# Kernel tuning notes

Hardware: AMD Instinct MI355X
Metric: run time of the kernel (lower is better)

Reference implementation:

```python
import jax, jax.numpy as jnp
import numpy as np

DIM = 1024
NUM_HEADS = 16
HEAD_DIM = DIM // NUM_HEADS
SCALE = HEAD_DIM ** -0.5
CAUSAL = True


def setup_inputs() -> dict:
    key = jax.random.key(0)
    k_x, k_qkv, k_proj, k_pb = jax.random.split(key, 4)
    B, S = 4, 2048
    x = jax.random.normal(k_x, (B, S, DIM), dtype=jnp.float32)
    # nn.Linear(dim, 3*dim, bias=False): weight [3*dim, dim]; store transposed [dim, 3*dim]
    w_qkv = jax.random.normal(k_qkv, (DIM, 3 * DIM), dtype=jnp.float32) * (DIM ** -0.5)
    w_proj = jax.random.normal(k_proj, (DIM, DIM), dtype=jnp.float32) * (DIM ** -0.5)
    b_proj = jax.random.normal(k_pb, (DIM,), dtype=jnp.float32) * 0.01
    return {"x": x, "w_qkv": w_qkv, "w_proj": w_proj, "b_proj": b_proj}


def reference(x, w_qkv, w_proj, b_proj):
    B, S, C = x.shape
    # qkv: [B, S, 3, H, D] -> q,k,v each [B, H, S, D]
    qkv = (x @ w_qkv).reshape(B, S, 3, NUM_HEADS, HEAD_DIM)
    qkv = jnp.transpose(qkv, (2, 0, 3, 1, 4))
    q, k, v = qkv[0], qkv[1], qkv[2]
    # scores [B, H, S, S]
    attn = jnp.einsum('bhqd,bhkd->bhqk', q, k) * SCALE
    if CAUSAL:
        causal_mask = jnp.triu(jnp.ones((S, S), dtype=bool), k=1)
        attn = jnp.where(causal_mask, -jnp.inf, attn)
    attn = jax.nn.softmax(attn, axis=-1)
    out = jnp.einsum('bhqk,bhkd->bhqd', attn, v)
    out = jnp.transpose(out, (0, 2, 1, 3)).reshape(B, S, C)
    return out @ w_proj + b_proj
```

## Files before the change

### kernel.cpp

```cpp
#include <hip/hip_runtime.h>
#include <hip/hip_bf16.h>
#include <math.h>

#define DIMC 1024
#define NHEADS 16
#define HDIM 64
#define BATCH 4
#define SEQ 2048
#define NROWS (BATCH * SEQ)
#define ATTN_SCALE 0.125f
#define LOG2E 1.4426950408889634f

typedef __attribute__((ext_vector_type(8))) short short8;
typedef __attribute__((ext_vector_type(4))) short short4v;
typedef __attribute__((ext_vector_type(4))) float f32x4;

static __device__ __forceinline__ short f2bf(float f) {
    __hip_bfloat16 h = __float2bfloat16(f);
    return *reinterpret_cast<short*>(&h);
}

static __device__ __forceinline__ void gload16(const void* g, void* l) {
    __builtin_amdgcn_global_load_lds(
        (const __attribute__((address_space(1))) unsigned int*)g,
        (__attribute__((address_space(3))) unsigned int*)l, 16, 0, 0);
}

__global__ __launch_bounds__(256)
void xcvt(const float* __restrict__ in, unsigned short* __restrict__ out) {
    int i = blockIdx.x * 256 + threadIdx.x;
    const float4* p = reinterpret_cast<const float4*>(in) + 2 * i;
    float4 a = p[0], b = p[1];
    short8 pk;
    pk[0] = f2bf(a.x); pk[1] = f2bf(a.y); pk[2] = f2bf(a.z); pk[3] = f2bf(a.w);
    pk[4] = f2bf(b.x); pk[5] = f2bf(b.y); pk[6] = f2bf(b.z); pk[7] = f2bf(b.w);
    reinterpret_cast<short8*>(out)[i] = pk;
}

__global__ __launch_bounds__(256)
void transpose_cvt(const float* __restrict__ src, unsigned short* __restrict__ dst,
                   int N) {
    __shared__ float t[64][65];
    const int tid = threadIdx.x;
    const int cb = blockIdx.x * 64;
    const int rb = blockIdx.y * 64;
#pragma unroll
    for (int e = 0; e < 4; e++) {
        int idx = tid + e * 256;
        int row = idx >> 4;
        int c4 = (idx & 15) << 2;
        *reinterpret_cast<float4*>(&t[row][c4]) =
            *reinterpret_cast<const float4*>(&src[(size_t)(rb + row) * N + cb + c4]);
    }
    __syncthreads();
#pragma unroll
    for (int e = 0; e < 2; e++) {
        int idx = tid + e * 256;
        int col = idx >> 3;
        int k8 = (idx & 7) << 3;
        short8 pk;
#pragma unroll
        for (int j = 0; j < 8; j++) pk[j] = f2bf(t[k8 + j][col]);
        *reinterpret_cast<short8*>(&dst[(size_t)(cb + col) * 1024 + rb + k8]) = pk;
    }
}

__global__ __launch_bounds__(256)
void qkv_gemm_mfma(const unsigned short* __restrict__ Xbf,
                   const unsigned short* __restrict__ Wt,
                   unsigned short* __restrict__ qo, unsigned short* __restrict__ ko,
                   unsigned short* __restrict__ vt) {
    __shared__ short Alds[128][64];
    __shared__ short Blds[128][64];
    const int tid = threadIdx.x;
    const int lane = tid & 63;
    const int wave = tid >> 6;
    const int wr = wave >> 1, wc = wave & 1;
    const int rowbase = blockIdx.y * 128;
    const int colbase = blockIdx.x * 128;
    const int g = lane >> 4, li = lane & 15;
    const int sr = lane >> 3;
    const int sc = ((lane & 7) ^ sr) * 8;
    const int swk = li & 7;
    short* aflat = &Alds[0][0];
    short* bflat = &Blds[0][0];

    f32x4 acc[4][4];
#pragma unroll
    for (int m = 0; m < 4; m++)
#pragma unroll
        for (int n = 0; n < 4; n++) acc[m][n] = (f32x4){0.f, 0.f, 0.f, 0.f};

    for (int k0 = 0; k0 < DIMC; k0 += 64) {
#pragma unroll
        for (int e = 0; e < 4; e++) {
            int j = wave * 4 + e;
            gload16(&Xbf[(size_t)(rowbase + j * 8 + sr) * DIMC + k0 + sc],
                    aflat + j * 512);
            gload16(&Wt[(size_t)(colbase + j * 8 + sr) * 1024 + k0 + sc],
                    bflat + j * 512);
        }
        __syncthreads();
#pragma unroll
        for (int ks = 0; ks < 2; ks++) {
            short8 af[4], bfr[4];
#pragma unroll
            for (int m = 0; m < 4; m++)
                af[m] = *reinterpret_cast<const short8*>(
                    &Alds[wr * 64 + m * 16 + li][((ks * 4 + g) ^ swk) * 8]);
#pragma unroll
            for (int n = 0; n < 4; n++)
                bfr[n] = *reinterpret_cast<const short8*>(
                    &Blds[wc * 64 + n * 16 + li][((ks * 4 + g) ^ swk) * 8]);
#pragma unroll
            for (int m = 0; m < 4; m++)
#pragma unroll
                for (int n = 0; n < 4; n++)
                    acc[m][n] = __builtin_amdgcn_mfma_f32_16x16x32_bf16(
                        af[m], bfr[n], acc[m][n], 0, 0, 0);
        }
        __syncthreads();
    }

    const int col0 = colbase + wc * 64;
    const int three = col0 >> 10;
    const int h = (col0 & 1023) >> 6;
    if (three < 2) {
        unsigned short* dst = (three == 0) ? qo : ko;
        const float mult = (three == 0) ? (ATTN_SCALE * LOG2E) : 1.0f;
#pragma unroll
        for (int n = 0; n < 4; n++) {
            int d = n * 16 + li;
#pragma unroll
            for (int m = 0; m < 4; m++) {
                int r0 = rowbase + wr * 64 + m * 16 + g * 4;
                int b = r0 >> 11;
                size_t base = ((size_t)(b * NHEADS + h) * SEQ) * HDIM + d;
#pragma unroll
                for (int r = 0; r < 4; r++) {
                    int s = (r0 + r) & 2047;
                    dst[base + (size_t)s * HDIM] = (unsigned short)f2bf(acc[m][n][r] * mult);
                }
            }
        }
    } else {
#pragma unroll
        for (int n = 0; n < 4; n++) {
            int d = n * 16 + li;
#pragma unroll
            for (int m = 0; m < 4; m++) {
                int r0 = rowbase + wr * 64 + m * 16 + g * 4;
                int b = r0 >> 11, s0 = r0 & 2047;
                short4v pk;
#pragma unroll
                for (int r = 0; r < 4; r++) pk[r] = f2bf(acc[m][n][r]);
                *reinterpret_cast<short4v*>(
                    &vt[((size_t)(b * NHEADS + h) * HDIM + d) * SEQ + s0]) = pk;
            }
        }
    }
}

__global__ __launch_bounds__(256)
void proj_gemm_mfma(const unsigned short* __restrict__ Abf,
                    const unsigned short* __restrict__ Wt,
                    const float* __restrict__ bias, float* __restrict__ out) {
    __shared__ short Alds[128][64];
    __shared__ short Blds[128][64];
    const int tid = threadIdx.x;
    const int lane = tid & 63;
    const int wave = tid >> 6;
    const int wr = wave >> 1, wc = wave & 1;
    const int rowbase = blockIdx.y * 128;
    const int colbase = blockIdx.x * 128;
    const int g = lane >> 4, li = lane & 15;
    const int sr = lane >> 3;
    const int sc = ((lane & 7) ^ sr) * 8;
    const int swk = li & 7;
    short* aflat = &Alds[0][0];
    short* bflat = &Blds[0][0];

    f32x4 acc[4][4];
#pragma unroll
    for (int m = 0; m < 4; m++)
#pragma unroll
        for (int n = 0; n < 4; n++) acc[m][n] = (f32x4){0.f, 0.f, 0.f, 0.f};

    for (int k0 = 0; k0 < DIMC; k0 += 64) {
#pragma unroll
        for (int e = 0; e < 4; e++) {
            int j = wave * 4 + e;
            gload16(&Abf[(size_t)(rowbase + j * 8 + sr) * DIMC + k0 + sc],
                    aflat + j * 512);
            gload16(&Wt[(size_t)(colbase + j * 8 + sr) * 1024 + k0 + sc],
                    bflat + j * 512);
        }
        __syncthreads();
#pragma unroll
        for (int ks = 0; ks < 2; ks++) {
            short8 af[4], bfr[4];
#pragma unroll
            for (int m = 0; m < 4; m++)
                af[m] = *reinterpret_cast<const short8*>(
                    &Alds[wr * 64 + m * 16 + li][((ks * 4 + g) ^ swk) * 8]);
#pragma unroll
            for (int n = 0; n < 4; n++)
                bfr[n] = *reinterpret_cast<const short8*>(
                    &Blds[wc * 64 + n * 16 + li][((ks * 4 + g) ^ swk) * 8]);
#pragma unroll
            for (int m = 0; m < 4; m++)
#pragma unroll
                for (int n = 0; n < 4; n++)
                    acc[m][n] = __builtin_amdgcn_mfma_f32_16x16x32_bf16(
                        af[m], bfr[n], acc[m][n], 0, 0, 0);
        }
        __syncthreads();
    }

#pragma unroll
    for (int n = 0; n < 4; n++) {
        int col = colbase + wc * 64 + n * 16 + li;
        float bv = bias[col];
#pragma unroll
        for (int m = 0; m < 4; m++) {
            int r0 = rowbase + wr * 64 + m * 16 + g * 4;
#pragma unroll
            for (int r = 0; r < 4; r++)
                out[(size_t)(r0 + r) * DIMC + col] = acc[m][n][r] + bv;
        }
    }
}

__global__ __launch_bounds__(512)
void flash_attn_mfma(const unsigned short* __restrict__ qg,
                     const unsigned short* __restrict__ kg,
                     const unsigned short* __restrict__ vt,
                     unsigned short* __restrict__ og) {
    __shared__ short Klds[2][64][64];
    __shared__ short Vlds[2][64][64];
    const int tid = threadIdx.x;
    const int lane = tid & 63;
    const int w = tid >> 6;
    const int g = lane >> 4, li = lane & 15;
    const int orig = blockIdx.x;
    const int swz = (orig & 7) * 64 + (orig >> 3);
    const int bx = swz & 7;
    const int bh = swz >> 3;
    const size_t head = (size_t)bh * SEQ * HDIM;
    const int b = bh >> 4, h = bh & 15;

    const int c0r = tid >> 3, c0c = tid & 7;

    const int abase0 = 8 * (li >> 2) + (li & 3);
    const int abase1 = abase0 + 4;

    for (int pass = 0; pass < 2; pass++) {
        const int qtile = pass ? (15 - bx) : bx;
        const int qbase = qtile * 128;
        const int qw = qbase + w * 16;
        const int nt = 2 * qtile + 2;

        short8 bq[2];
#pragma unroll
        for (int ds = 0; ds < 2; ds++)
            bq[ds] = *reinterpret_cast<const short8*>(
                &qg[head + (size_t)(qw + li) * HDIM + ds * 32 + g * 8]);

        f32x4 accO[4];
#pragma unroll
        for (int df = 0; df < 4; df++) accO[df] = (f32x4){0.f, 0.f, 0.f, 0.f};
        float mrow = -INFINITY;
        float lrow = 0.f;

        const unsigned short* kp = kg + head + (size_t)c0r * HDIM + c0c * 8;
        const unsigned short* vp = vt + head + (size_t)c0r * SEQ + c0c * 8;

        short8 kreg, vreg;
        kreg = *reinterpret_cast<const short8*>(kp);
        vreg = *reinterpret_cast<const short8*>(vp);
        kp += 64 * HDIM; vp += 64;
        {
            const int sw0 = (c0c ^ (c0r & 7)) * 8;
            *reinterpret_cast<short8*>(&Klds[0][c0r][sw0]) = kreg;
            *reinterpret_cast<short8*>(&Vlds[0][c0r][sw0]) = vreg;
        }
        __syncthreads();

        for (int t = 0; t < nt; t++) {
            const int kvbase = t * 64;
            const int buf = t & 1;
            const bool more = (t + 1 < nt);
            if (more) {
                kreg = *reinterpret_cast<const short8*>(kp);
                vreg = *reinterpret_cast<const short8*>(vp);
                kp += 64 * HDIM; vp += 64;
            }

            if (kvbase <= qw + 15) {
                f32x4 s[4];
#pragma unroll
                for (int m = 0; m < 4; m++) s[m] = (f32x4){0.f, 0.f, 0.f, 0.f};
#pragma unroll
                for (int ds = 0; ds < 2; ds++) {
                    short8 ak[4];
#pragma unroll
                    for (int m = 0; m < 4; m++) {
                        int arow = 32 * (m >> 1) + ((m & 1) ? abase1 : abase0);
                        ak[m] = *reinterpret_cast<const short8*>(
                            &Klds[buf][arow][((ds * 4 + g) ^ (arow & 7)) * 8]);
                    }
                    __builtin_amdgcn_s_setprio(1);
#pragma unroll
                    for (int m = 0; m < 4; m++)
                        s[m] = __builtin_amdgcn_mfma_f32_16x16x32_bf16(
                            ak[m], bq[ds], s[m], 0, 0, 0);
                    __builtin_amdgcn_s_setprio(0);
                }
                const bool diag = (kvbase + 63 > qw);
                if (diag) {
                    int q = qw + li;
#pragma unroll
                    for (int m = 0; m < 4; m++) {
                        int kv0 = kvbase + 32 * (m >> 1) + 8 * g + 4 * (m & 1);
#pragma unroll
                        for (int r = 0; r < 4; r++)
                            if (kv0 + r > q) s[m][r] = -INFINITY;
                    }
                }
                float a0 = fmaxf(fmaxf(s[0][0], s[0][1]), fmaxf(s[0][2], s[0][3]));
                float a1 = fmaxf(fmaxf(s[1][0], s[1][1]), fmaxf(s[1][2], s[1][3]));
                float a2 = fmaxf(fmaxf(s[2][0], s[2][1]), fmaxf(s[2][2], s[2][3]));
                float a3 = fmaxf(fmaxf(s[3][0], s[3][1]), fmaxf(s[3][2], s[3][3]));
                float tm = fmaxf(fmaxf(a0, a1), fmaxf(a2, a3));
                tm = fmaxf(tm, __shfl_xor(tm, 16));
                tm = fmaxf(tm, __shfl_xor(tm, 32));
                float mnew = fmaxf(mrow, tm);
                float corr = __builtin_amdgcn_exp2f(mrow - mnew);
                mrow = mnew;
                float p[4][4];
                float sm[4];
#pragma unroll
                for (int m = 0; m < 4; m++) {
#pragma unroll
                    for (int r = 0; r < 4; r++)
                        p[m][r] = __builtin_amdgcn_exp2f(s[m][r] - mrow);
                    sm[m] = (p[m][0] + p[m][1]) + (p[m][2] + p[m][3]);
                }
                short8 bp[2];
#pragma unroll
                for (int ks = 0; ks < 2; ks++) {
                    unsigned u0 = (__float_as_uint(p[2 * ks][1]) & 0xFFFF0000u) |
                                  (__float_as_uint(p[2 * ks][0]) >> 16);
                    unsigned u1 = (__float_as_uint(p[2 * ks][3]) & 0xFFFF0000u) |
                                  (__float_as_uint(p[2 * ks][2]) >> 16);
                    unsigned u2 = (__float_as_uint(p[2 * ks + 1][1]) & 0xFFFF0000u) |
                                  (__float_as_uint(p[2 * ks + 1][0]) >> 16);
                    unsigned u3 = (__float_as_uint(p[2 * ks + 1][3]) & 0xFFFF0000u) |
                                  (__float_as_uint(p[2 * ks + 1][2]) >> 16);
                    unsigned q4[4] = {u0, u1, u2, u3};
                    bp[ks] = *reinterpret_cast<short8*>(q4);
                }
                float ts = (sm[0] + sm[1]) + (sm[2] + sm[3]);
                ts += __shfl_xor(ts, 16);
                ts += __shfl_xor(ts, 32);
                lrow = lrow * corr + ts;
                if (!__all((int)(corr == 1.0f))) {
#pragma unroll
                    for (int df = 0; df < 4; df++) {
                        accO[df][0] *= corr; accO[df][1] *= corr;
                        accO[df][2] *= corr; accO[df][3] *= corr;
                    }
                }
#pragma unroll
                for (int ks = 0; ks < 2; ks++) {
                    short8 av[4];
#pragma unroll
                    for (int df = 0; df < 4; df++) {
                        int vrow = li + 16 * df;
                        av[df] = *reinterpret_cast<const short8*>(
                            &Vlds[buf][vrow][((ks * 4 + g) ^ (vrow & 7)) * 8]);
                    }
                    __builtin_amdgcn_s_setprio(1);
#pragma unroll
                    for (int df = 0; df < 4; df++)
                        accO[df] = __builtin_amdgcn_mfma_f32_16x16x32_bf16(
                            av[df], bp[ks], accO[df], 0, 0, 0);
                    __builtin_amdgcn_s_setprio(0);
                }
            }

            if (more) {
                const int nbuf = buf ^ 1;
                const int sw0 = (c0c ^ (c0r & 7)) * 8;
                *reinterpret_cast<short8*>(&Klds[nbuf][c0r][sw0]) = kreg;
                *reinterpret_cast<short8*>(&Vlds[nbuf][c0r][sw0]) = vreg;
            }
            __syncthreads();
        }

        {
            float inv = 1.0f / lrow;
            int q = qw + li;
            size_t rowoff = (size_t)(b * SEQ + q) * DIMC + h * HDIM;
#pragma unroll
            for (int df = 0; df < 4; df++) {
                short4v pk;
#pragma unroll
                for (int r = 0; r < 4; r++) pk[r] = f2bf(accO[df][r] * inv);
                *reinterpret_cast<short4v*>(&og[rowoff + 16 * df + 4 * g]) = pk;
            }
        }
        __syncthreads();
    }
}

extern "C" void kernel_launch(void* const* d_in, const int* in_sizes, int n_in,
                              void* d_out, int out_size, void* d_ws, size_t ws_size,
                              hipStream_t stream) {
    const float* x      = (const float*)d_in[0];
    const float* w_qkv  = (const float*)d_in[1];
    const float* w_proj = (const float*)d_in[2];
    const float* b_proj = (const float*)d_in[3];
    float* out = (float*)d_out;

    char* w = (char*)d_ws;
    unsigned short* qb  = (unsigned short*)(w);
    unsigned short* kb  = (unsigned short*)(w + ((size_t)16 << 20));
    unsigned short* vtb = (unsigned short*)(w + ((size_t)32 << 20));
    unsigned short* ao  = (unsigned short*)(w + ((size_t)48 << 20));
    unsigned short* wqt = (unsigned short*)(w + ((size_t)64 << 20));
    unsigned short* wpt = (unsigned short*)(w + ((size_t)72 << 20));
    unsigned short* xbf = (unsigned short*)(w + ((size_t)80 << 20));

    xcvt<<<NROWS * DIMC / (256 * 8), 256, 0, stream>>>(x, xbf);
    transpose_cvt<<<dim3(3 * DIMC / 64, DIMC / 64), 256, 0, stream>>>(w_qkv, wqt, 3 * DIMC);
    transpose_cvt<<<dim3(DIMC / 64, DIMC / 64), 256, 0, stream>>>(w_proj, wpt, DIMC);
    qkv_gemm_mfma<<<dim3(3 * DIMC / 128, NROWS / 128), 256, 0, stream>>>(xbf, wqt, qb, kb, vtb);
    flash_attn_mfma<<<512, 512, 0, stream>>>(qb, kb, vtb, ao);
    proj_gemm_mfma<<<dim3(DIMC / 128, NROWS / 128), 256, 0, stream>>>(ao, wpt, b_proj, out);
}
```

Baseline: 247.6 us.

## Double-buffer GEMM LDS tiles with interleaved prefetch and merge prep kernels

Both projection GEMMs now use two LDS buffers. The loads for the next K-tile are issued in four pieces interleaved between MFMA groups, with explicit vmcnt waits and raw s_barrier, and MFMA sections run at raised wave priority. This is meant to hide global-to-LDS latency behind compute and cut one barrier's stall per iteration, at the cost of doubling LDS per block, which can lower occupancy. Separately, the three input-conversion kernels are fused into one launch to remove launch overhead.

Result: slower. 291.7 us (+17.8%).

```diff
diff --git a/kernel.cpp b/kernel.cpp
--- a/kernel.cpp
+++ b/kernel.cpp
@@ -27,23 +27,27 @@
 }
 
 __global__ __launch_bounds__(256)
-void xcvt(const float* __restrict__ in, unsigned short* __restrict__ out) {
-    int i = blockIdx.x * 256 + threadIdx.x;
-    const float4* p = reinterpret_cast<const float4*>(in) + 2 * i;
-    float4 a = p[0], b = p[1];
-    short8 pk;
-    pk[0] = f2bf(a.x); pk[1] = f2bf(a.y); pk[2] = f2bf(a.z); pk[3] = f2bf(a.w);
-    pk[4] = f2bf(b.x); pk[5] = f2bf(b.y); pk[6] = f2bf(b.z); pk[7] = f2bf(b.w);
-    reinterpret_cast<short8*>(out)[i] = pk;
-}
-
-__global__ __launch_bounds__(256)
-void transpose_cvt(const float* __restrict__ src, unsigned short* __restrict__ dst,
-                   int N) {
+void prep(const float* __restrict__ x, unsigned short* __restrict__ xbf,
+          const float* __restrict__ wq, unsigned short* __restrict__ wqt,
+          const float* __restrict__ wp, unsigned short* __restrict__ wpt) {
+    const int tid = threadIdx.x;
+    int blk = blockIdx.x;
+    if (blk < 4096) {
+        int i = blk * 256 + tid;
+        const float4* p = reinterpret_cast<const float4*>(x) + 2 * i;
+        float4 a = p[0], b = p[1];
+        short8 pk;
+        pk[0] = f2bf(a.x); pk[1] = f2bf(a.y); pk[2] = f2bf(a.z); pk[3] = f2bf(a.w);
+        pk[4] = f2bf(b.x); pk[5] = f2bf(b.y); pk[6] = f2bf(b.z); pk[7] = f2bf(b.w);
+        reinterpret_cast<short8*>(xbf)[i] = pk;
+        return;
+    }
+    blk -= 4096;
+    const float* src; unsigned short* dst; int N, cb, rb;
+    if (blk < 768) { src = wq; dst = wqt; N = 3072; cb = (blk % 48) * 64; rb = (blk / 48) * 64; }
+    else { blk -= 768; src = wp; dst = wpt; N = 1024; cb = (blk % 16) * 64; rb = (blk / 16) * 64; }
+
     __shared__ float t[64][65];
-    const int tid = threadIdx.x;
-    const int cb = blockIdx.x * 64;
-    const int rb = blockIdx.y * 64;
 #pragma unroll
     for (int e = 0; e < 4; e++) {
         int idx = tid + e * 256;
@@ -65,13 +69,22 @@
     }
 }
 
+#define GEMM_STAGE(SRC_A, SRC_B, LDB, e, k0n, bu)                               \
+    {                                                                           \
+        int j_ = wave * 4 + (e);                                                \
+        gload16(&SRC_A[(size_t)(rowbase + j_ * 8 + sr) * DIMC + (k0n) + sc],    \
+                &Alds[bu][0][0] + j_ * 512);                                    \
+        gload16(&SRC_B[(size_t)(colbase + j_ * 8 + sr) * (LDB) + (k0n) + sc],   \
+                &Blds[bu][0][0] + j_ * 512);                                    \
+    }
+
 __global__ __launch_bounds__(256)
 void qkv_gemm_mfma(const unsigned short* __restrict__ Xbf,
                    const unsigned short* __restrict__ Wt,
                    unsigned short* __restrict__ qo, unsigned short* __restrict__ ko,
                    unsigned short* __restrict__ vt) {
-    __shared__ short Alds[128][64];
-    __shared__ short Blds[128][64];
+    __shared__ short Alds[2][128][64];
+    __shared__ short Blds[2][128][64];
     const int tid = threadIdx.x;
     const int lane = tid & 63;
     const int wave = tid >> 6;
@@ -82,8 +95,6 @@
     const int sr = lane >> 3;
     const int sc = ((lane & 7) ^ sr) * 8;
     const int swk = li & 7;
-    short* aflat = &Alds[0][0];
-    short* bflat = &Blds[0][0];
 
     f32x4 acc[4][4];
 #pragma unroll
@@ -91,35 +102,83 @@
 #pragma unroll
         for (int n = 0; n < 4; n++) acc[m][n] = (f32x4){0.f, 0.f, 0.f, 0.f};
 
-    for (int k0 = 0; k0 < DIMC; k0 += 64) {
-#pragma unroll
-        for (int e = 0; e < 4; e++) {
-            int j = wave * 4 + e;
-            gload16(&Xbf[(size_t)(rowbase + j * 8 + sr) * DIMC + k0 + sc],
-                    aflat + j * 512);
-            gload16(&Wt[(size_t)(colbase + j * 8 + sr) * 1024 + k0 + sc],
-                    bflat + j * 512);
-        }
-        __syncthreads();
-#pragma unroll
-        for (int ks = 0; ks < 2; ks++) {
-            short8 af[4], bfr[4];
-#pragma unroll
-            for (int m = 0; m < 4; m++)
-                af[m] = *reinterpret_cast<const short8*>(
-                    &Alds[wr * 64 + m * 16 + li][((ks * 4 + g) ^ swk) * 8]);
-#pragma unroll
-            for (int n = 0; n < 4; n++)
-                bfr[n] = *reinterpret_cast<const short8*>(
-                    &Blds[wc * 64 + n * 16 + li][((ks * 4 + g) ^ swk) * 8]);
-#pragma unroll
-            for (int m = 0; m < 4; m++)
-#pragma unroll
-                for (int n = 0; n < 4; n++)
-                    acc[m][n] = __builtin_amdgcn_mfma_f32_16x16x32_bf16(
-                        af[m], bfr[n], acc[m][n], 0, 0, 0);
-        }
-        __syncthreads();
+#pragma unroll
+    for (int e = 0; e < 4; e++) GEMM_STAGE(Xbf, Wt, 1024, e, 0, 0);
+
+    for (int t = 0; t < 16; t++) {
+        const int buf = t & 1;
+        const int nbuf = buf ^ 1;
+        const int nk0 = (t + 1) * 64;
+        const bool more = (t < 15);
+        if (more) {
+            GEMM_STAGE(Xbf, Wt, 1024, 0, nk0, nbuf);
+            asm volatile("s_waitcnt vmcnt(2)" ::: "memory");
+        } else {
+            asm volatile("s_waitcnt vmcnt(0)" ::: "memory");
+        }
+        asm volatile("s_barrier" ::: "memory");
+
+        short8 af[4], bfr[2];
+#pragma unroll
+        for (int m = 0; m < 4; m++)
+            af[m] = *reinterpret_cast<const short8*>(
+                &Alds[buf][wr * 64 + m * 16 + li][((0 + g) ^ swk) * 8]);
+#pragma unroll
+        for (int n = 0; n < 2; n++)
+            bfr[n] = *reinterpret_cast<const short8*>(
+                &Blds[buf][wc * 64 + n * 16 + li][((0 + g) ^ swk) * 8]);
+        __builtin_amdgcn_s_setprio(1);
+#pragma unroll
+        for (int m = 0; m < 4; m++)
+#pragma unroll
+            for (int n = 0; n < 2; n++)
+                acc[m][n] = __builtin_amdgcn_mfma_f32_16x16x32_bf16(
+                    af[m], bfr[n], acc[m][n], 0, 0, 0);
+        __builtin_amdgcn_s_setprio(0);
+        if (more) GEMM_STAGE(Xbf, Wt, 1024, 1, nk0, nbuf);
+#pragma unroll
+        for (int n = 0; n < 2; n++)
+            bfr[n] = *reinterpret_cast<const short8*>(
+                &Blds[buf][wc * 64 + (n + 2) * 16 + li][((0 + g) ^ swk) * 8]);
+        __builtin_amdgcn_s_setprio(1);
+#pragma unroll
+        for (int m = 0; m < 4; m++)
+#pragma unroll
+            for (int n = 0; n < 2; n++)
+                acc[m][n + 2] = __builtin_amdgcn_mfma_f32_16x16x32_bf16(
+                    af[m], bfr[n], acc[m][n + 2], 0, 0, 0);
+        __builtin_amdgcn_s_setprio(0);
+        if (more) GEMM_STAGE(Xbf, Wt, 1024, 2, nk0, nbuf);
+#pragma unroll
+        for (int m = 0; m < 4; m++)
+            af[m] = *reinterpret_cast<const short8*>(
+                &Alds[buf][wr * 64 + m * 16 + li][((4 + g) ^ swk) * 8]);
+#pragma unroll
+        for (int n = 0; n < 2; n++)
+            bfr[n] = *reinterpret_cast<const short8*>(
+                &Blds[buf][wc * 64 + n * 16 + li][((4 + g) ^ swk) * 8]);
+        __builtin_amdgcn_s_setprio(1);
+#pragma unroll
+        for (int m = 0; m < 4; m++)
+#pragma unroll
+            for (int n = 0; n < 2; n++)
+                acc[m][n] = __builtin_amdgcn_mfma_f32_16x16x32_bf16(
+                    af[m], bfr[n], acc[m][n], 0, 0, 0);
+        __builtin_amdgcn_s_setprio(0);
+        if (more) GEMM_STAGE(Xbf, Wt, 1024, 3, nk0, nbuf);
+#pragma unroll
+        for (int n = 0; n < 2; n++)
+            bfr[n] = *reinterpret_cast<const short8*>(
+                &Blds[buf][wc * 64 + (n + 2) * 16 + li][((4 + g) ^ swk) * 8]);
+        __builtin_amdgcn_s_setprio(1);
+#pragma unroll
+        for (int m = 0; m < 4; m++)
+#pragma unroll
+            for (int n = 0; n < 2; n++)
+                acc[m][n + 2] = __builtin_amdgcn_mfma_f32_16x16x32_bf16(
+                    af[m], bfr[n], acc[m][n + 2], 0, 0, 0);
+        __builtin_amdgcn_s_setprio(0);
+        asm volatile("s_barrier" ::: "memory");
     }
 
     const int col0 = colbase + wc * 64;
@@ -165,8 +224,8 @@
 void proj_gemm_mfma(const unsigned short* __restrict__ Abf,
                     const unsigned short* __restrict__ Wt,
                     const float* __restrict__ bias, float* __restrict__ out) {
-    __shared__ short Alds[128][64];
-    __shared__ short Blds[128][64];
+    __shared__ short Alds[2][128][64];
+    __shared__ short Blds[2][128][64];
     const int tid = threadIdx.x;
     const int lane = tid & 63;
     const int wave = tid >> 6;
@@ -177,8 +236,6 @@
     const int sr = lane >> 3;
     const int sc = ((lane & 7) ^ sr) * 8;
     const int swk = li & 7;
-    short* aflat = &Alds[0][0];
-    short* bflat = &Blds[0][0];
 
     f32x4 acc[4][4];
 #pragma unroll
@@ -186,35 +243,83 @@
 #pragma unroll
         for (int n = 0; n < 4; n++) acc[m][n] = (f32x4){0.f, 0.f, 0.f, 0.f};
 
-    for (int k0 = 0; k0 < DIMC; k0 += 64) {
-#pragma unroll
-        for (int e = 0; e < 4; e++) {
-            int j = wave * 4 + e;
-            gload16(&Abf[(size_t)(rowbase + j * 8 + sr) * DIMC + k0 + sc],
-                    aflat + j * 512);
-            gload16(&Wt[(size_t)(colbase + j * 8 + sr) * 1024 + k0 + sc],
-                    bflat + j * 512);
-        }
-        __syncthreads();
-#pragma unroll
-        for (int ks = 0; ks < 2; ks++) {
-            short8 af[4], bfr[4];
-#pragma unroll
-            for (int m = 0; m < 4; m++)
-                af[m] = *reinterpret_cast<const short8*>(
-                    &Alds[wr * 64 + m * 16 + li][((ks * 4 + g) ^ swk) * 8]);
-#pragma unroll
-            for (int n = 0; n < 4; n++)
-                bfr[n] = *reinterpret_cast<const short8*>(
-                    &Blds[wc * 64 + n * 16 + li][((ks * 4 + g) ^ swk) * 8]);
-#pragma unroll
-            for (int m = 0; m < 4; m++)
-#pragma unroll
-                for (int n = 0; n < 4; n++)
-                    acc[m][n] = __builtin_amdgcn_mfma_f32_16x16x32_bf16(
-                        af[m], bfr[n], acc[m][n], 0, 0, 0);
-        }
-        __syncthreads();
+#pragma unroll
+    for (int e = 0; e < 4; e++) GEMM_STAGE(Abf, Wt, 1024, e, 0, 0);
+
+    for (int t = 0; t < 16; t++) {
+        const int buf = t & 1;
+        const int nbuf = buf ^ 1;
+        const int nk0 = (t + 1) * 64;
+        const bool more = (t < 15);
+        if (more) {
+            GEMM_STAGE(Abf, Wt, 1024, 0, nk0, nbuf);
+            asm volatile("s_waitcnt vmcnt(2)" ::: "memory");
+        } else {
+            asm volatile("s_waitcnt vmcnt(0)" ::: "memory");
+        }
+        asm volatile("s_barrier" ::: "memory");
+
+        short8 af[4], bfr[2];
+#pragma unroll
+        for (int m = 0; m < 4; m++)
+            af[m] = *reinterpret_cast<const short8*>(
+                &Alds[buf][wr * 64 + m * 16 + li][((0 + g) ^ swk) * 8]);
+#pragma unroll
+        for (int n = 0; n < 2; n++)
+            bfr[n] = *reinterpret_cast<const short8*>(
+                &Blds[buf][wc * 64 + n * 16 + li][((0 + g) ^ swk) * 8]);
+        __builtin_amdgcn_s_setprio(1);
+#pragma unroll
+        for (int m = 0; m < 4; m++)
+#pragma unroll
+            for (int n = 0; n < 2; n++)
+                acc[m][n] = __builtin_amdgcn_mfma_f32_16x16x32_bf16(
+                    af[m], bfr[n], acc[m][n], 0, 0, 0);
+        __builtin_amdgcn_s_setprio(0);
+        if (more) GEMM_STAGE(Abf, Wt, 1024, 1, nk0, nbuf);
+#pragma unroll
+        for (int n = 0; n < 2; n++)
+            bfr[n] = *reinterpret_cast<const short8*>(
+                &Blds[buf][wc * 64 + (n + 2) * 16 + li][((0 + g) ^ swk) * 8]);
+        __builtin_amdgcn_s_setprio(1);
+#pragma unroll
+        for (int m = 0; m < 4; m++)
+#pragma unroll
+            for (int n = 0; n < 2; n++)
+                acc[m][n + 2] = __builtin_amdgcn_mfma_f32_16x16x32_bf16(
+                    af[m], bfr[n], acc[m][n + 2], 0, 0, 0);
+        __builtin_amdgcn_s_setprio(0);
+        if (more) GEMM_STAGE(Abf, Wt, 1024, 2, nk0, nbuf);
+#pragma unroll
+        for (int m = 0; m < 4; m++)
+            af[m] = *reinterpret_cast<const short8*>(
+                &Alds[buf][wr * 64 + m * 16 + li][((4 + g) ^ swk) * 8]);
+#pragma unroll
+        for (int n = 0; n < 2; n++)
+            bfr[n] = *reinterpret_cast<const short8*>(
+                &Blds[buf][wc * 64 + n * 16 + li][((4 + g) ^ swk) * 8]);
+        __builtin_amdgcn_s_setprio(1);
+#pragma unroll
+        for (int m = 0; m < 4; m++)
+#pragma unroll
+            for (int n = 0; n < 2; n++)
+                acc[m][n] = __builtin_amdgcn_mfma_f32_16x16x32_bf16(
+                    af[m], bfr[n], acc[m][n], 0, 0, 0);
+        __builtin_amdgcn_s_setprio(0);
+        if (more) GEMM_STAGE(Abf, Wt, 1024, 3, nk0, nbuf);
+#pragma unroll
+        for (int n = 0; n < 2; n++)
+            bfr[n] = *reinterpret_cast<const short8*>(
+                &Blds[buf][wc * 64 + (n + 2) * 16 + li][((4 + g) ^ swk) * 8]);
+        __builtin_amdgcn_s_setprio(1);
+#pragma unroll
+        for (int m = 0; m < 4; m++)
+#pragma unroll
+            for (int n = 0; n < 2; n++)
+                acc[m][n + 2] = __builtin_amdgcn_mfma_f32_16x16x32_bf16(
+                    af[m], bfr[n], acc[m][n + 2], 0, 0, 0);
+        __builtin_amdgcn_s_setprio(0);
+        asm volatile("s_barrier" ::: "memory");
     }
 
 #pragma unroll
@@ -432,9 +537,7 @@
     unsigned short* wpt = (unsigned short*)(w + ((size_t)72 << 20));
     unsigned short* xbf = (unsigned short*)(w + ((size_t)80 << 20));
 
-    xcvt<<<NROWS * DIMC / (256 * 8), 256, 0, stream>>>(x, xbf);
-    transpose_cvt<<<dim3(3 * DIMC / 64, DIMC / 64), 256, 0, stream>>>(w_qkv, wqt, 3 * DIMC);
-    transpose_cvt<<<dim3(DIMC / 64, DIMC / 64), 256, 0, stream>>>(w_proj, wpt, DIMC);
+    prep<<<4096 + 768 + 256, 256, 0, stream>>>(x, xbf, w_qkv, wqt, w_proj, wpt);
     qkv_gemm_mfma<<<dim3(3 * DIMC / 128, NROWS / 128), 256, 0, stream>>>(xbf, wqt, qb, kb, vtb);
     flash_attn_mfma<<<512, 512, 0, stream>>>(qb, kb, vtb, ao);
     proj_gemm_mfma<<<dim3(DIMC / 128, NROWS / 128), 256, 0, stream>>>(ao, wpt, b_proj, out);
```
